# Performance work log

Hardware: AMD Instinct MI355X
Metric: run time of the kernel (lower is better)

The kernel has to match this reference:

```python
import jax, jax.numpy as jnp
import numpy as np

B, T, D, H = 2, 2048, 1024, 16
HD = D // H  # head_dim = 64


def apply_rope(x, cos, sin):
    # x: [B, H, T, HD]; cos/sin: [1, 1, T, HD//2]
    x1, x2 = x[..., ::2], x[..., 1::2]
    y1 = x1 * cos - x2 * sin
    y2 = x1 * sin + x2 * cos
    # interleave back: [..., HD//2, 2] -> [..., HD]
    return jnp.stack([y1, y2], axis=-1).reshape(x.shape)


def setup_inputs() -> dict:
    key = jax.random.key(0)
    ks = jax.random.split(key, 11)
    s = 0.02
    return {
        "x": jax.random.normal(ks[0], (B, T, D), jnp.float32),
        "cos": jax.random.normal(ks[1], (1, 1, T, HD // 2), jnp.float32),
        "sin": jax.random.normal(ks[2], (1, 1, T, HD // 2), jnp.float32),
        "Wq": jax.random.normal(ks[3], (D, D), jnp.float32) * s,
        "bq": jax.random.normal(ks[4], (D,), jnp.float32) * s,
        "Wk": jax.random.normal(ks[5], (D, D), jnp.float32) * s,
        "bk": jax.random.normal(ks[6], (D,), jnp.float32) * s,
        "Wv": jax.random.normal(ks[7], (D, D), jnp.float32) * s,
        "bv": jax.random.normal(ks[8], (D,), jnp.float32) * s,
        "Wo": jax.random.normal(ks[9], (D, D), jnp.float32) * s,
        "bo": jax.random.normal(ks[10], (D,), jnp.float32) * s,
    }


def reference(x, cos, sin, Wq, bq, Wk, bk, Wv, bv, Wo, bo):
    b, t, d = x.shape
    # projections (nn.Linear: x @ W.T + b)
    q = (x @ Wq.T + bq).reshape(b, t, H, HD).transpose(0, 2, 1, 3)
    k = (x @ Wk.T + bk).reshape(b, t, H, HD).transpose(0, 2, 1, 3)
    v = (x @ Wv.T + bv).reshape(b, t, H, HD).transpose(0, 2, 1, 3)
    q = apply_rope(q, cos, sin)
    k = apply_rope(k, cos, sin)
    scores = jnp.einsum("bhqd,bhkd->bhqk", q, k) / jnp.sqrt(jnp.asarray(HD, x.dtype))
    # causal mask: query i attends to keys j <= i
    causal = jnp.tril(jnp.ones((t, t), dtype=bool))
    scores = jnp.where(causal, scores, jnp.asarray(-jnp.inf, x.dtype))
    weights = jax.nn.softmax(scores, axis=-1)
    out = jnp.einsum("bhqk,bhkd->bhqd", weights, v)
    out = out.transpose(0, 2, 1, 3).reshape(b, t, d)
    return out @ Wo.T + bo
```

## Files before the change

kernel.cpp:

```cpp
#include <hip/hip_runtime.h>
#include <hip/hip_bf16.h>
#include <cstdint>
#include <cstddef>

typedef __attribute__((ext_vector_type(8))) short bf16x8;
typedef __attribute__((ext_vector_type(4))) float f32x4;
typedef __attribute__((ext_vector_type(16))) float f32x16;

#define SCALE2 0.180336880111112f
#define VSTRIDE 2080

__device__ __forceinline__ unsigned short f2bf(float f) {
    unsigned u = __builtin_bit_cast(unsigned, f);
    unsigned r = (u + 0x7FFFu + ((u >> 16) & 1u)) >> 16;
    return (unsigned short)r;
}

__device__ __forceinline__ void gload16(const unsigned short* g, unsigned short* l) {
    __builtin_amdgcn_global_load_lds(
        (const __attribute__((address_space(1))) unsigned int*)(g),
        (__attribute__((address_space(3))) unsigned int*)(l), 16, 0, 0);
}

__global__ void cvt_all(const float* __restrict__ x,
                        const float* __restrict__ wq, const float* __restrict__ wk,
                        const float* __restrict__ wv, const float* __restrict__ wo,
                        unsigned short* __restrict__ xb,
                        unsigned short* __restrict__ wqb, unsigned short* __restrict__ wkb,
                        unsigned short* __restrict__ wvb, unsigned short* __restrict__ wob)
{
    const int y = blockIdx.y;
    const float* src; unsigned short* dst; int n;
    switch (y) {
        case 0: src = x;  dst = xb;  n = 4194304; break;
        case 1: src = wq; dst = wqb; n = 1048576; break;
        case 2: src = wk; dst = wkb; n = 1048576; break;
        case 3: src = wv; dst = wvb; n = 1048576; break;
        default: src = wo; dst = wob; n = 1048576; break;
    }
    const int i = (blockIdx.x * 256 + threadIdx.x) * 4;
    if (i < n) {
        float4 v = *(const float4*)(src + i);
        ushort4 o;
        o.x = f2bf(v.x); o.y = f2bf(v.y); o.z = f2bf(v.z); o.w = f2bf(v.w);
        *(ushort4*)(dst + i) = o;
    }
}

__global__ __launch_bounds__(512) void gemm_qkv(
    const unsigned short* __restrict__ xb,
    const unsigned short* __restrict__ wqb,
    const unsigned short* __restrict__ wkb,
    const unsigned short* __restrict__ wvb,
    const float* __restrict__ bq, const float* __restrict__ bk, const float* __restrict__ bv,
    const float* __restrict__ cosT, const float* __restrict__ sinT,
    unsigned short* __restrict__ Qb, unsigned short* __restrict__ Kb, unsigned short* __restrict__ Vtg)
{
    const int bid = blockIdx.x;
    const int xcd = bid & 7;
    const int s = bid >> 3;
    const int i4 = xcd >> 1, k2 = xcd & 1;
    const int z = s >> 5;
    const int tt = s & 31;
    const int m0 = (i4 * 8 + (tt >> 2)) * 128;
    const int n0 = (k2 * 4 + (tt & 3)) * 128;

    const unsigned short* wb = (z == 0) ? wqb : ((z == 1) ? wkb : wvb);
    const float* bias = (z == 0) ? bq : ((z == 1) ? bk : bv);
    unsigned short* dst = (z == 0) ? Qb : Kb;

    __shared__ __align__(16) unsigned short Al[128 * 32];
    __shared__ __align__(16) unsigned short Bl[128 * 32];
    __shared__ __align__(16) unsigned short Ct[128 * 136];

    const int tid = threadIdx.x;
    const int lane = tid & 63;
    const int w = tid >> 6;
    const int wr = w >> 2, wc = w & 3;
    const int lr = lane & 15, lg = lane >> 4;
    const int srow = tid >> 2, sseg = tid & 3;
    const int ldst = (tid & ~63) * 8;

    f32x4 acc[4][2] = {};

    for (int k0 = 0; k0 < 1024; k0 += 32) {
        __syncthreads();
        gload16(xb + (size_t)(m0 + srow) * 1024 + k0 + sseg * 8, Al + ldst);
        gload16(wb + (size_t)(n0 + srow) * 1024 + k0 + sseg * 8, Bl + ldst);
        __syncthreads();
        bf16x8 af[4], bfr[2];
#pragma unroll
        for (int mt = 0; mt < 4; ++mt)
            af[mt] = *(const bf16x8*)(Al + (wr * 64 + mt * 16 + lr) * 32 + lg * 8);
#pragma unroll
        for (int nt = 0; nt < 2; ++nt)
            bfr[nt] = *(const bf16x8*)(Bl + (wc * 32 + nt * 16 + lr) * 32 + lg * 8);
#pragma unroll
        for (int mt = 0; mt < 4; ++mt)
#pragma unroll
            for (int nt = 0; nt < 2; ++nt)
                acc[mt][nt] = __builtin_amdgcn_mfma_f32_16x16x32_bf16(af[mt], bfr[nt], acc[mt][nt], 0, 0, 0);
    }

#pragma unroll
    for (int mt = 0; mt < 4; ++mt) {
#pragma unroll
        for (int nt = 0; nt < 2; ++nt) {
            const int coln = wc * 32 + nt * 16 + lr;
            const int col = n0 + coln;
            const float bcol = bias[col];
            const int hd = col & 63;
#pragma unroll
            for (int r = 0; r < 4; ++r) {
                const int rowm = wr * 64 + mt * 16 + lg * 4 + r;
                float v = acc[mt][nt][r] + bcol;
                if (z < 2) {
                    float part = __shfl_xor(v, 1);
                    const int ttm = (m0 + rowm) & 2047;
                    const int i = hd >> 1;
                    const float cc = cosT[ttm * 32 + i], ss = sinT[ttm * 32 + i];
                    v = (hd & 1) ? (part * ss + v * cc) : (v * cc - part * ss);
                    if (z == 0) v *= SCALE2;
                    Ct[rowm * 136 + coln] = f2bf(v);
                } else {
                    Ct[coln * 136 + rowm] = f2bf(v);
                }
            }
        }
    }
    __syncthreads();
    if (z < 2) {
#pragma unroll
        for (int p = 0; p < 4; ++p) {
            const int u = p * 512 + tid;
            const int row = u >> 4, seg = u & 15;
            bf16x8 vv = *(const bf16x8*)(Ct + row * 136 + seg * 8);
            const int mrow = m0 + row;
            const int ttm = mrow & 2047, bb = mrow >> 11;
            const int col = n0 + seg * 8;
            const int h = col >> 6, hd = col & 63;
            *(bf16x8*)(dst + ((size_t)(bb * 16 + h) * 2048 + ttm) * 64 + hd) = vv;
        }
    } else {
        const int bb = m0 >> 11;
#pragma unroll
        for (int p = 0; p < 4; ++p) {
            const int u = p * 512 + tid;
            const int vrow = u >> 4, seg = u & 15;
            bf16x8 vv = *(const bf16x8*)(Ct + vrow * 136 + seg * 8);
            const int col = n0 + vrow;
            const int h = col >> 6, hd = col & 63;
            const int ttm = (m0 + seg * 8) & 2047;
            *(bf16x8*)(Vtg + ((size_t)(bb * 16 + h) * 64 + hd) * VSTRIDE + ttm) = vv;
        }
    }
}

__global__ __launch_bounds__(512) void attn_fwd(
    const unsigned short* __restrict__ Qb, const unsigned short* __restrict__ Kb,
    const unsigned short* __restrict__ Vtg, unsigned short* __restrict__ attnb)
{
    __shared__ __align__(16) unsigned char smem[49152];

    const int tid = threadIdx.x, lane = tid & 63, w = tid >> 6;
    const int l31 = lane & 31, lh = lane >> 5;
    const int bid = blockIdx.x;
    const int bh = bid & 31;
    const int g = bid >> 5;
    const int cidx = w >> 1;
    const int slice = w & 1;
    const int c = (cidx == 0) ? (63 - g) : ((cidx == 1) ? (47 - g) : ((cidx == 2) ? (16 + g) : g));
    const int smax = (63 - g) >> 1;
    const size_t base = (size_t)bh * 131072;
    const int myq = c * 32 + l31;

    const unsigned short* Kg = Kb + base;
    const unsigned short* Vg = Vtg + (size_t)bh * (64 * VSTRIDE);

    bf16x8 qf[4];
#pragma unroll
    for (int s = 0; s < 4; ++s)
        qf[s] = *(const bf16x8*)(Qb + base + (size_t)myq * 64 + s * 16 + lh * 8);

    f32x16 o0 = {}, o1 = {};
    float sm = 0.f;

#define STAGE(S, B)                                                                   \
    {                                                                                 \
        unsigned short* kb_ = (unsigned short*)(smem + (B) * 16384);                  \
        unsigned short* vb_ = (unsigned short*)(smem + (B) * 16384 + 8192);           \
        const int row = tid >> 3, ss = (tid & 7) ^ (row & 7);                         \
        gload16(Kg + (size_t)((S) * 64 + row) * 64 + ss * 8, kb_ + (tid & ~63) * 8);  \
        gload16(Vg + (size_t)row * VSTRIDE + (S) * 64 + ss * 8, vb_ + (tid & ~63) * 8);\
    }

    STAGE(0, 0);
    STAGE(1, 1);
    int bsel = 0;
    for (int s = 0; s <= smax; ++s) {
        if (s < smax) asm volatile("s_waitcnt vmcnt(2)" ::: "memory");
        else          asm volatile("s_waitcnt vmcnt(0)" ::: "memory");
        __syncthreads();
        if (s + 2 <= smax) {
            int b2 = bsel + 2; if (b2 >= 3) b2 -= 3;
            STAGE(s + 2, b2);
        }
        const int t = 2 * s + slice;
        if (t <= c) {
            const unsigned short* Kc = (const unsigned short*)(smem + bsel * 16384);
            const unsigned short* Vc = Kc + 4096;
            const int kvb = t * 32;
            const int sw = l31 & 7;
            const int roff = slice * 32 + l31;

            bf16x8 kf0 = *(const bf16x8*)(Kc + roff * 64 + ((0 + lh) ^ sw) * 8);
            bf16x8 kf1 = *(const bf16x8*)(Kc + roff * 64 + ((2 + lh) ^ sw) * 8);
            bf16x8 kf2 = *(const bf16x8*)(Kc + roff * 64 + ((4 + lh) ^ sw) * 8);
            bf16x8 kf3 = *(const bf16x8*)(Kc + roff * 64 + ((6 + lh) ^ sw) * 8);

            f32x16 st = {};
            st = __builtin_amdgcn_mfma_f32_32x32x16_bf16(kf0, qf[0], st, 0, 0, 0);
            st = __builtin_amdgcn_mfma_f32_32x32x16_bf16(kf1, qf[1], st, 0, 0, 0);
            st = __builtin_amdgcn_mfma_f32_32x32x16_bf16(kf2, qf[2], st, 0, 0, 0);
            st = __builtin_amdgcn_mfma_f32_32x32x16_bf16(kf3, qf[3], st, 0, 0, 0);

            if (t == c) {
#pragma unroll
                for (int r = 0; r < 16; ++r) {
                    const int kv = kvb + (r & 3) + 8 * (r >> 2) + 4 * lh;
                    st[r] = (kv <= myq) ? st[r] : -1e30f;
                }
            }
#pragma unroll
            for (int r = 0; r < 16; ++r) st[r] = exp2f(st[r]);
            {
                float a0 = st[0] + st[1], a1 = st[2] + st[3];
                float a2 = st[4] + st[5], a3 = st[6] + st[7];
                float a4 = st[8] + st[9], a5 = st[10] + st[11];
                float a6 = st[12] + st[13], a7 = st[14] + st[15];
                sm += ((a0 + a1) + (a2 + a3)) + ((a4 + a5) + (a6 + a7));
            }

            unsigned pw0, pw1, pw2, pw3, pw4, pw5, pw6, pw7;
            {
                unsigned a0, a1, b0, b1;
                asm("v_cvt_pk_bf16_f32 %0, %1, %2" : "=v"(a0) : "v"(st[0]), "v"(st[1]));
                asm("v_cvt_pk_bf16_f32 %0, %1, %2" : "=v"(a1) : "v"(st[2]), "v"(st[3]));
                asm("v_cvt_pk_bf16_f32 %0, %1, %2" : "=v"(b0) : "v"(st[4]), "v"(st[5]));
                asm("v_cvt_pk_bf16_f32 %0, %1, %2" : "=v"(b1) : "v"(st[6]), "v"(st[7]));
                asm("v_permlane32_swap_b32 %0, %1" : "+v"(a0), "+v"(b0));
                asm("v_permlane32_swap_b32 %0, %1" : "+v"(a1), "+v"(b1));
                pw0 = a0; pw1 = a1; pw2 = b0; pw3 = b1;
            }
            {
                unsigned a0, a1, b0, b1;
                asm("v_cvt_pk_bf16_f32 %0, %1, %2" : "=v"(a0) : "v"(st[8]), "v"(st[9]));
                asm("v_cvt_pk_bf16_f32 %0, %1, %2" : "=v"(a1) : "v"(st[10]), "v"(st[11]));
                asm("v_cvt_pk_bf16_f32 %0, %1, %2" : "=v"(b0) : "v"(st[12]), "v"(st[13]));
                asm("v_cvt_pk_bf16_f32 %0, %1, %2" : "=v"(b1) : "v"(st[14]), "v"(st[15]));
                asm("v_permlane32_swap_b32 %0, %1" : "+v"(a0), "+v"(b0));
                asm("v_permlane32_swap_b32 %0, %1" : "+v"(a1), "+v"(b1));
                pw4 = a0; pw5 = a1; pw6 = b0; pw7 = b1;
            }

            const int vs0 = (slice * 4 + lh) ^ sw;
            const int vs1 = (slice * 4 + 2 + lh) ^ sw;
            bf16x8 vf00 = *(const bf16x8*)(Vc + l31 * 64 + vs0 * 8);
            bf16x8 vf01 = *(const bf16x8*)(Vc + l31 * 64 + vs1 * 8);
            bf16x8 vf10 = *(const bf16x8*)(Vc + (32 + l31) * 64 + vs0 * 8);
            bf16x8 vf11 = *(const bf16x8*)(Vc + (32 + l31) * 64 + vs1 * 8);

            uint4 h0 = make_uint4(pw0, pw1, pw2, pw3);
            uint4 h1 = make_uint4(pw4, pw5, pw6, pw7);
            bf16x8 pf0 = __builtin_bit_cast(bf16x8, h0);
            bf16x8 pf1 = __builtin_bit_cast(bf16x8, h1);
            o0 = __builtin_amdgcn_mfma_f32_32x32x16_bf16(vf00, pf0, o0, 0, 0, 0);
            o1 = __builtin_amdgcn_mfma_f32_32x32x16_bf16(vf10, pf0, o1, 0, 0, 0);
            o0 = __builtin_amdgcn_mfma_f32_32x32x16_bf16(vf01, pf1, o0, 0, 0, 0);
            o1 = __builtin_amdgcn_mfma_f32_32x32x16_bf16(vf11, pf1, o1, 0, 0, 0);
        }
        bsel += 1; if (bsel == 3) bsel = 0;
    }

    sm += __shfl_xor(sm, 32);

    float* Om = (float*)smem;
    float* Ms = (float*)(smem + 32768);
    __syncthreads();
    if (slice == 1) {
#pragma unroll
        for (int i = 0; i < 16; ++i) Om[(cidx * 32 + i) * 64 + lane] = o0[i];
#pragma unroll
        for (int i = 0; i < 16; ++i) Om[(cidx * 32 + 16 + i) * 64 + lane] = o1[i];
        Ms[cidx * 64 + lane] = sm;
    }
    __syncthreads();
    if (slice == 0) {
        const float s = sm + Ms[cidx * 64 + lane];
        const float inv = 1.f / s;
        const int b = bh >> 4, h = bh & 15;
        unsigned short* obase = attnb + ((size_t)(b * 2048 + myq)) * 1024 + h * 64;
#pragma unroll
        for (int gg = 0; gg < 4; ++gg) {
            ushort4 u;
            u.x = f2bf((o0[gg * 4 + 0] + Om[(cidx * 32 + gg * 4 + 0) * 64 + lane]) * inv);
            u.y = f2bf((o0[gg * 4 + 1] + Om[(cidx * 32 + gg * 4 + 1) * 64 + lane]) * inv);
            u.z = f2bf((o0[gg * 4 + 2] + Om[(cidx * 32 + gg * 4 + 2) * 64 + lane]) * inv);
            u.w = f2bf((o0[gg * 4 + 3] + Om[(cidx * 32 + gg * 4 + 3) * 64 + lane]) * inv);
            *(ushort4*)(obase + gg * 8 + lh * 4) = u;
            ushort4 v;
            v.x = f2bf((o1[gg * 4 + 0] + Om[(cidx * 32 + 16 + gg * 4 + 0) * 64 + lane]) * inv);
            v.y = f2bf((o1[gg * 4 + 1] + Om[(cidx * 32 + 16 + gg * 4 + 1) * 64 + lane]) * inv);
            v.z = f2bf((o1[gg * 4 + 2] + Om[(cidx * 32 + 16 + gg * 4 + 2) * 64 + lane]) * inv);
            v.w = f2bf((o1[gg * 4 + 3] + Om[(cidx * 32 + 16 + gg * 4 + 3) * 64 + lane]) * inv);
            *(ushort4*)(obase + 32 + gg * 8 + lh * 4) = v;
        }
    }
#undef STAGE
}

__global__ __launch_bounds__(256) void gemm_out(
    const unsigned short* __restrict__ ab,
    const unsigned short* __restrict__ wob,
    const float* __restrict__ bo,
    float* __restrict__ out)
{
    __shared__ __align__(16) unsigned short Al[128 * 32];
    __shared__ __align__(16) unsigned short Bl[64 * 32];

    const int bid = blockIdx.x;
    const int xcd = bid & 7;
    const int s = bid >> 3;
    const int i4 = xcd >> 1, k2 = xcd & 1;
    const int m0 = (i4 * 8 + (s >> 3)) * 128;
    const int n0 = (k2 * 8 + (s & 7)) * 64;

    const int tid = threadIdx.x;
    const int lane = tid & 63;
    const int w = tid >> 6;
    const int lr = lane & 15, lg = lane >> 4;

    f32x4 acc[2][4] = {};

    for (int k0 = 0; k0 < 1024; k0 += 32) {
        __syncthreads();
#pragma unroll
        for (int p = 0; p < 2; ++p) {
            const int u = p * 256 + tid;
            const int row = u >> 2, seg = u & 3;
            gload16(ab + (size_t)(m0 + row) * 1024 + k0 + seg * 8, Al + (u & ~63) * 8);
        }
        {
            const int u = tid;
            const int row = u >> 2, seg = u & 3;
            gload16(wob + (size_t)(n0 + row) * 1024 + k0 + seg * 8, Bl + (u & ~63) * 8);
        }
        __syncthreads();
        bf16x8 af[2], bfr[4];
#pragma unroll
        for (int mt = 0; mt < 2; ++mt)
            af[mt] = *(const bf16x8*)(Al + (w * 32 + mt * 16 + lr) * 32 + lg * 8);
#pragma unroll
        for (int nt = 0; nt < 4; ++nt)
            bfr[nt] = *(const bf16x8*)(Bl + (nt * 16 + lr) * 32 + lg * 8);
#pragma unroll
        for (int mt = 0; mt < 2; ++mt)
#pragma unroll
            for (int nt = 0; nt < 4; ++nt)
                acc[mt][nt] = __builtin_amdgcn_mfma_f32_16x16x32_bf16(af[mt], bfr[nt], acc[mt][nt], 0, 0, 0);
    }

#pragma unroll
    for (int mt = 0; mt < 2; ++mt) {
#pragma unroll
        for (int nt = 0; nt < 4; ++nt) {
            const int col = n0 + nt * 16 + lr;
            const float bcol = bo[col];
#pragma unroll
            for (int r = 0; r < 4; ++r) {
                const int mrow = m0 + w * 32 + mt * 16 + lg * 4 + r;
                out[(size_t)mrow * 1024 + col] = acc[mt][nt][r] + bcol;
            }
        }
    }
}

extern "C" void kernel_launch(void* const* d_in, const int* in_sizes, int n_in,
                              void* d_out, int out_size, void* d_ws, size_t ws_size,
                              hipStream_t stream) {
    const float* x    = (const float*)d_in[0];
    const float* cosT = (const float*)d_in[1];
    const float* sinT = (const float*)d_in[2];
    const float* Wq   = (const float*)d_in[3];
    const float* bq   = (const float*)d_in[4];
    const float* Wk   = (const float*)d_in[5];
    const float* bk   = (const float*)d_in[6];
    const float* Wv   = (const float*)d_in[7];
    const float* bv   = (const float*)d_in[8];
    const float* Wo   = (const float*)d_in[9];
    const float* bo   = (const float*)d_in[10];
    float* out = (float*)d_out;

    char* ws = (char*)d_ws;
    unsigned short* xb    = (unsigned short*)(ws + 0);
    unsigned short* attnb = (unsigned short*)(ws + 0);
    unsigned short* wob   = (unsigned short*)(ws + 8388608);
    unsigned short* wqb   = (unsigned short*)(ws + 10485760);
    unsigned short* wkb   = (unsigned short*)(ws + 12582912);
    unsigned short* wvb   = (unsigned short*)(ws + 14680064);
    unsigned short* Qb    = (unsigned short*)(ws + 16777216);
    unsigned short* Kb    = (unsigned short*)(ws + 25165824);
    unsigned short* Vtg   = (unsigned short*)(ws + 33554432);

    cvt_all<<<dim3(4096, 5), 256, 0, stream>>>(x, Wq, Wk, Wv, Wo, xb, wqb, wkb, wvb, wob);
    gemm_qkv<<<dim3(768), 512, 0, stream>>>(xb, wqb, wkb, wvb, bq, bk, bv,
                                            cosT, sinT, Qb, Kb, Vtg);
    attn_fwd<<<dim3(512), 512, 0, stream>>>(Qb, Kb, Vtg, attnb);
    gemm_out<<<dim3(512), 256, 0, stream>>>(attnb, wob, bo, out);
}
```

Before: 108.6 us.

## Triple-buffer QKV projection GEMM loads and XOR-swizzle LDS tiles

The QKV projection GEMM now uses a three-stage LDS ring buffer. Global-to-LDS loads for k-step kk+2 are issued while step kk computes, guarded by explicit vmcnt waits, and one barrier per iteration replaces the previous two. The 16-byte segment slot in each LDS row is also XOR-swizzled by row to reduce bank conflicts on fragment reads. The epilogue staging buffer now reuses the same shared allocation after a barrier. LDS use stays about the same, but the hand-written waitcnt logic is fragile.

```diff
diff --git a/kernel.cpp b/kernel.cpp
--- a/kernel.cpp
+++ b/kernel.cpp
@@ -69,39 +69,61 @@
     const float* bias = (z == 0) ? bq : ((z == 1) ? bk : bv);
     unsigned short* dst = (z == 0) ? Qb : Kb;
 
-    __shared__ __align__(16) unsigned short Al[128 * 32];
-    __shared__ __align__(16) unsigned short Bl[128 * 32];
-    __shared__ __align__(16) unsigned short Ct[128 * 136];
+    __shared__ __align__(16) unsigned char gsm[49152];
 
     const int tid = threadIdx.x;
     const int lane = tid & 63;
     const int w = tid >> 6;
     const int wr = w >> 2, wc = w & 3;
     const int lr = lane & 15, lg = lane >> 4;
-    const int srow = tid >> 2, sseg = tid & 3;
-    const int ldst = (tid & ~63) * 8;
+    const int srow = tid >> 2;
+    const int sslot = (tid & 3) ^ (srow & 3);
+    const int wdst = (tid & ~63) * 8;
 
     f32x4 acc[4][2] = {};
 
-    for (int k0 = 0; k0 < 1024; k0 += 32) {
+#define GSTAGE(KK, B)                                                                  \
+    {                                                                                  \
+        unsigned short* ab_ = (unsigned short*)(gsm + (B) * 16384);                    \
+        unsigned short* bb_ = ab_ + 4096;                                              \
+        gload16(xb + (size_t)(m0 + srow) * 1024 + (KK) * 32 + sslot * 8, ab_ + wdst);  \
+        gload16(wb + (size_t)(n0 + srow) * 1024 + (KK) * 32 + sslot * 8, bb_ + wdst);  \
+    }
+
+    GSTAGE(0, 0);
+    GSTAGE(1, 1);
+    int bsel = 0;
+    for (int kk = 0; kk < 32; ++kk) {
+        if (kk < 31) asm volatile("s_waitcnt vmcnt(2)" ::: "memory");
+        else         asm volatile("s_waitcnt vmcnt(0)" ::: "memory");
         __syncthreads();
-        gload16(xb + (size_t)(m0 + srow) * 1024 + k0 + sseg * 8, Al + ldst);
-        gload16(wb + (size_t)(n0 + srow) * 1024 + k0 + sseg * 8, Bl + ldst);
-        __syncthreads();
+        if (kk + 2 < 32) {
+            int b2 = bsel + 2; if (b2 >= 3) b2 -= 3;
+            GSTAGE(kk + 2, b2);
+        }
+        const unsigned short* Al = (const unsigned short*)(gsm + bsel * 16384);
+        const unsigned short* Bl = Al + 4096;
         bf16x8 af[4], bfr[2];
 #pragma unroll
-        for (int mt = 0; mt < 4; ++mt)
-            af[mt] = *(const bf16x8*)(Al + (wr * 64 + mt * 16 + lr) * 32 + lg * 8);
-#pragma unroll
-        for (int nt = 0; nt < 2; ++nt)
-            bfr[nt] = *(const bf16x8*)(Bl + (wc * 32 + nt * 16 + lr) * 32 + lg * 8);
+        for (int mt = 0; mt < 4; ++mt) {
+            const int row = wr * 64 + mt * 16 + lr;
+            af[mt] = *(const bf16x8*)(Al + row * 32 + (lg ^ (row & 3)) * 8);
+        }
+#pragma unroll
+        for (int nt = 0; nt < 2; ++nt) {
+            const int row = wc * 32 + nt * 16 + lr;
+            bfr[nt] = *(const bf16x8*)(Bl + row * 32 + (lg ^ (row & 3)) * 8);
+        }
 #pragma unroll
         for (int mt = 0; mt < 4; ++mt)
 #pragma unroll
             for (int nt = 0; nt < 2; ++nt)
                 acc[mt][nt] = __builtin_amdgcn_mfma_f32_16x16x32_bf16(af[mt], bfr[nt], acc[mt][nt], 0, 0, 0);
-    }
-
+        bsel += 1; if (bsel == 3) bsel = 0;
+    }
+
+    unsigned short* Ct = (unsigned short*)gsm;
+    __syncthreads();
 #pragma unroll
     for (int mt = 0; mt < 4; ++mt) {
 #pragma unroll
@@ -154,6 +176,7 @@
             *(bf16x8*)(Vtg + ((size_t)(bb * 16 + h) * 64 + hd) * VSTRIDE + ttm) = vv;
         }
     }
+#undef GSTAGE
 }
 
 __global__ __launch_bounds__(512) void attn_fwd(
```

Measured after the change: 108.5 us. No clear change (-0.1%).
